# Performance work log

Hardware: AMD Instinct MI355X
Metric: run time of the kernel (lower is better)

Reference implementation:

```python
import jax, jax.numpy as jnp
import numpy as np

B, S, D, H, DFF = 2, 2048, 1024, 16, 4096
DK = D // H
EPS = 1e-6


def setup_inputs() -> dict:
    key = jax.random.key(0)
    ks = jax.random.split(key, 12)
    p = lambda k, shp: (jax.random.normal(k, shp, dtype=jnp.float32) * 0.02)
    return {
        "x": jax.random.normal(ks[0], (B, S, D), dtype=jnp.float32),
        "src_mask": jax.random.randint(ks[1], (B, 1, 1, S), 0, 2, dtype=jnp.int32),
        "wq": p(ks[2], (D, D)), "bq": jnp.zeros((D,), jnp.float32),
        "wk": p(ks[3], (D, D)), "bk": jnp.zeros((D,), jnp.float32),
        "wv": p(ks[4], (D, D)), "bv": jnp.zeros((D,), jnp.float32),
        "wo": p(ks[5], (D, D)), "bo": jnp.zeros((D,), jnp.float32),
        "w1": p(ks[6], (D, DFF)), "b1": jnp.zeros((DFF,), jnp.float32),
        "w2": p(ks[7], (DFF, D)), "b2": jnp.zeros((D,), jnp.float32),
        "a1": jnp.ones((1,), jnp.float32), "g1": jnp.zeros((1,), jnp.float32),
        "a2": jnp.ones((1,), jnp.float32), "g2": jnp.zeros((1,), jnp.float32),
    }


def _layernorm(x, alpha, bias):
    # Faithful to source: scalar alpha/bias, std with Bessel correction, eps on std
    mean = jnp.mean(x, axis=-1, keepdims=True)
    std = jnp.std(x, axis=-1, keepdims=True, ddof=1)
    return alpha * (x - mean) / (std + EPS) + bias


def _encoder_block(x, src_mask, wq, bq, wk, bk, wv, bv, wo, bo,
                   w1, b1, w2, b2, a1, g1, a2, g2):
    # --- self-attention sublayer (pre-norm residual) ---
    n = _layernorm(x, a1, g1)
    q = (n @ wq + bq).reshape(B, S, H, DK)
    k = (n @ wk + bk).reshape(B, S, H, DK)
    v = (n @ wv + bv).reshape(B, S, H, DK)
    scores = jnp.einsum("bqhd,bkhd->bhqk", q, k) / jnp.sqrt(jnp.float32(DK))
    scores = jnp.where(src_mask == 0, jnp.float32(-1e9), scores)
    attn = jax.nn.softmax(scores, axis=-1)
    ctx = jnp.einsum("bhqk,bkhd->bqhd", attn, v).reshape(B, S, D)
    x = x + (ctx @ wo + bo)
    # --- feed-forward sublayer (pre-norm residual) ---
    n2 = _layernorm(x, a2, g2)
    ff = jax.nn.relu(n2 @ w1 + b1) @ w2 + b2
    return x + ff


def reference(x, src_mask, wq, bq, wk, bk, wv, bv, wo, bo,
              w1, b1, w2, b2, a1, g1, a2, g2):
    return _encoder_block(x, src_mask, wq, bq, wk, bk, wv, bv, wo, bo,
                          w1, b1, w2, b2, a1, g1, a2, g2)
```

## Files before the change

### kernel.cpp

```cpp
#include <hip/hip_runtime.h>
#include <hip/hip_bf16.h>
#include <cstdint>

constexpr int Bc  = 2;
constexpr int Sc  = 2048;
constexpr int Dc  = 1024;
constexpr int Hc  = 16;
constexpr int DKc = 64;
constexpr int DFFc= 4096;
constexpr int BSc = Bc * Sc;

typedef __attribute__((ext_vector_type(8))) short bf16x8;
typedef __attribute__((ext_vector_type(4))) float f32x4;

__device__ __forceinline__ unsigned short f2bf(float x){
  union { float f; uint32_t u; } v; v.f = x;
  uint32_t r = v.u + 0x7fffu + ((v.u >> 16) & 1u);
  return (unsigned short)(r >> 16);
}

__device__ __forceinline__ void gload16(const void* g, void* l){
  __builtin_amdgcn_global_load_lds((const __attribute__((address_space(1))) void*)g,
                                   (__attribute__((address_space(3))) void*)l, 16, 0, 0);
}

__device__ __forceinline__ f32x4 mfma16(bf16x8 a, bf16x8 b, f32x4 c){
  return __builtin_amdgcn_mfma_f32_16x16x32_bf16(a, b, c, 0, 0, 0);
}

__device__ __forceinline__ uint32_t pk2bf(float lo, float hi){
  __hip_bfloat162 h = __float22bfloat162_rn(make_float2(lo, hi));
  return *reinterpret_cast<uint32_t*>(&h);
}

__device__ __forceinline__ float fexp2(float x){
  float r; asm("v_exp_f32 %0, %1" : "=v"(r) : "v"(x)); return r;
}

__device__ __forceinline__ int xcd_swz(int bid, int nwg){
  const int q = nwg >> 3, r = nwg & 7;
  const int xcd = bid & 7, idx = bid >> 3;
  return ((xcd < r) ? (xcd * (q + 1)) : (r * (q + 1) + (xcd - r) * q)) + idx;
}

__global__ __launch_bounds__(256)
void prep_all(const float* __restrict__ wq, const float* __restrict__ wk,
              const float* __restrict__ wv, const float* __restrict__ wo,
              const float* __restrict__ w1, const float* __restrict__ w2,
              const float* __restrict__ bq, const float* __restrict__ bk,
              const float* __restrict__ bv,
              unsigned short* __restrict__ wqkv_t, unsigned short* __restrict__ wo_t,
              unsigned short* __restrict__ w1_t, unsigned short* __restrict__ w2_t,
              float* __restrict__ bqkv,
              const float* __restrict__ x, const float* __restrict__ al,
              const float* __restrict__ be, unsigned short* __restrict__ nbuf){
  const int id = blockIdx.x, tid = threadIdx.x;
  if (id >= 12300){
    const int row = id - 12300;
    const float4 v = ((const float4*)(x + (long)row * Dc))[tid];
    float s  = v.x + v.y + v.z + v.w;
    float ss = v.x*v.x + v.y*v.y + v.z*v.z + v.w*v.w;
#pragma unroll
    for (int d = 1; d < 64; d <<= 1){ s += __shfl_xor(s, d, 64); ss += __shfl_xor(ss, d, 64); }
    __shared__ float red[8];
    const int wid = tid >> 6, lane = tid & 63;
    if (lane == 0){ red[wid*2] = s; red[wid*2+1] = ss; }
    __syncthreads();
    s  = red[0] + red[2] + red[4] + red[6];
    ss = red[1] + red[3] + red[5] + red[7];
    const float mean = s * (1.f / 1024.f);
    float var = (ss - s * mean) * (1.f / 1023.f);
    var = fmaxf(var, 0.f);
    const float k = al[0] / (sqrtf(var) + 1e-6f);
    const float g = be[0];
    ushort4 o;
    o.x = f2bf((v.x - mean) * k + g);
    o.y = f2bf((v.y - mean) * k + g);
    o.z = f2bf((v.z - mean) * k + g);
    o.w = f2bf((v.w - mean) * k + g);
    ((ushort4*)(nbuf + (long)row * Dc))[tid] = o;
    return;
  }
  if (id >= 12288){
    const int i = (id - 12288) * 256 + tid;
    bqkv[i] = (i < 1024) ? bq[i] : (i < 2048 ? bk[i - 1024] : bv[i - 2048]);
    return;
  }
  const float* in; unsigned short* out; int K, N, bx, by;
  if (id < 4096){
    const int w = id >> 10, local = id & 1023;
    in  = (w == 0) ? wq : (w == 1) ? wk : (w == 2) ? wv : wo;
    out = (w == 0) ? wqkv_t : (w == 1) ? (wqkv_t + 1048576) : (w == 2) ? (wqkv_t + 2097152) : wo_t;
    K = 1024; N = 1024; bx = local & 31; by = local >> 5;
  } else if (id < 8192){
    const int local = id - 4096;
    in = w1; out = w1_t; K = 1024; N = 4096; bx = local & 127; by = local >> 7;
  } else {
    const int local = id - 8192;
    in = w2; out = w2_t; K = 4096; N = 1024; bx = local & 31; by = local >> 5;
  }
  __shared__ float t[32][33];
  const int tx = tid & 31, ty = tid >> 5;
  const int x0 = bx * 32, y0 = by * 32;
#pragma unroll
  for (int j = ty; j < 32; j += 8) t[j][tx] = in[(long)(y0 + j) * N + x0 + tx];
  __syncthreads();
#pragma unroll
  for (int j = ty; j < 32; j += 8)
    out[(long)(x0 + j) * K + y0 + tx] = f2bf(t[tx][j]);
}

__global__ __launch_bounds__(256)
void layernorm_k(const float* __restrict__ x, const float* __restrict__ al,
                 const float* __restrict__ be, unsigned short* __restrict__ out){
  const int row = blockIdx.x, tid = threadIdx.x;
  const float4 v = ((const float4*)(x + (long)row * Dc))[tid];
  float s  = v.x + v.y + v.z + v.w;
  float ss = v.x*v.x + v.y*v.y + v.z*v.z + v.w*v.w;
#pragma unroll
  for (int d = 1; d < 64; d <<= 1){ s += __shfl_xor(s, d, 64); ss += __shfl_xor(ss, d, 64); }
  __shared__ float red[8];
  const int wid = tid >> 6, lane = tid & 63;
  if (lane == 0){ red[wid*2] = s; red[wid*2+1] = ss; }
  __syncthreads();
  s  = red[0] + red[2] + red[4] + red[6];
  ss = red[1] + red[3] + red[5] + red[7];
  const float mean = s * (1.f / 1024.f);
  float var = (ss - s * mean) * (1.f / 1023.f);
  var = fmaxf(var, 0.f);
  const float k = al[0] / (sqrtf(var) + 1e-6f);
  const float g = be[0];
  ushort4 o;
  o.x = f2bf((v.x - mean) * k + g);
  o.y = f2bf((v.y - mean) * k + g);
  o.z = f2bf((v.z - mean) * k + g);
  o.w = f2bf((v.w - mean) * k + g);
  ((ushort4*)(out + (long)row * Dc))[tid] = o;
}

template<int RELU, int OUTBF16, int RES, int VOUT>
__global__ __launch_bounds__(512, 2)
void gemm256(const unsigned short* __restrict__ A, const unsigned short* __restrict__ BT,
             const float* __restrict__ bias, const float* __restrict__ resid,
             void* __restrict__ Cout, unsigned short* __restrict__ vtw,
             int M, int N, int K){
  __shared__ unsigned short As[2][256 * 64];
  __shared__ unsigned short Bs[2][256 * 64];
  const int tid = threadIdx.x, wid = tid >> 6, lane = tid & 63;
  const int lg = lane >> 4, lr = lane & 15;
  const int wm = wid >> 2, wn = wid & 3;
  const int nwg = gridDim.x * gridDim.y;
  const int wg  = xcd_swz(blockIdx.y * gridDim.x + blockIdx.x, nwg);
  const int bx = wg % gridDim.x, by = wg / gridDim.x;
  const int m0 = by * 256, n0 = bx * 256;
  const long ldA = (long)K * 2;
  const f32x4 zero4 = {0.f, 0.f, 0.f, 0.f};
  f32x4 acc[8][4];
#pragma unroll
  for (int i = 0; i < 8; i++)
#pragma unroll
    for (int j = 0; j < 4; j++) acc[i][j] = zero4;

  auto stage_half = [&](int b, int kt, int h){
    const unsigned short* src = (h < 2) ? A : BT;
    const int rowg = ((h < 2) ? m0 : n0) + (h & 1) * 128;
    char* dst = ((h < 2) ? (char*)As[b] : (char*)Bs[b]) + (h & 1) * 16384;
#pragma unroll
    for (int l = 0; l < 2; ++l){
      const int ob = (wid*2 + l) * 1024;
      const int o  = ob + lane * 16;
      const int rr = o >> 7, c = (o >> 4) & 7;
      const long co = (long)kt * 128 + ((c ^ (rr & 7)) << 4);
      gload16((const char*)src + (long)(rowg + rr) * ldA + co, dst + ob);
    }
  };

  const int nt = K >> 6;
#pragma unroll
  for (int h = 0; h < 4; ++h) stage_half(0, 0, h);
  __syncthreads();

  int cur = 0;
  for (int t = 0; t < nt; ++t){
    const char* as = (const char*)As[cur];
    const char* bs = (const char*)Bs[cur];
    bf16x8 bfr[4][2];
#pragma unroll
    for (int p = 0; p < 4; ++p){
      if (p == 0){
#pragma unroll
        for (int ni = 0; ni < 4; ++ni){
          const int row = wn*64 + ni*16 + lr;
#pragma unroll
          for (int ks = 0; ks < 2; ++ks)
            bfr[ni][ks] = *reinterpret_cast<const bf16x8*>(bs + row*128 + (((ks*4 + lg) ^ (row & 7)) << 4));
        }
      }
      bf16x8 af[2][2];
#pragma unroll
      for (int i = 0; i < 2; ++i){
        const int arow = wm*128 + (2*p + i)*16 + lr;
        af[i][0] = *reinterpret_cast<const bf16x8*>(as + arow*128 + (((0*4 + lg) ^ (arow & 7)) << 4));
        af[i][1] = *reinterpret_cast<const bf16x8*>(as + arow*128 + (((1*4 + lg) ^ (arow & 7)) << 4));
      }
      if (t + 1 < nt) stage_half(cur ^ 1, t + 1, p);
      __builtin_amdgcn_sched_barrier(0);
      __builtin_amdgcn_s_barrier();
      asm volatile("s_waitcnt lgkmcnt(0)" ::: "memory");
      __builtin_amdgcn_sched_barrier(0);
      __builtin_amdgcn_s_setprio(1);
#pragma unroll
      for (int i = 0; i < 2; ++i){
        const int mi = 2*p + i;
#pragma unroll
        for (int ni = 0; ni < 4; ++ni){
          acc[mi][ni] = mfma16(af[i][0], bfr[ni][0], acc[mi][ni]);
          acc[mi][ni] = mfma16(af[i][1], bfr[ni][1], acc[mi][ni]);
        }
      }
      __builtin_amdgcn_s_setprio(0);
      __builtin_amdgcn_sched_barrier(0);
      __builtin_amdgcn_s_barrier();
    }
    if (t + 1 < nt){
      asm volatile("s_waitcnt vmcnt(0)" ::: "memory");
      __builtin_amdgcn_s_barrier();
      __builtin_amdgcn_sched_barrier(0);
    }
    cur ^= 1;
  }

  if (VOUT && n0 >= 2048){
#pragma unroll
    for (int mi = 0; mi < 8; ++mi){
      const int row = m0 + wm*128 + mi*16 + lg*4;
      const int b = row >> 11, s = row & 2047;
#pragma unroll
      for (int ni = 0; ni < 4; ++ni){
        const int col = n0 + wn*64 + ni*16 + lr;
        const float bc = bias[col];
        ushort4 o;
        o.x = f2bf(acc[mi][ni][0] + bc);
        o.y = f2bf(acc[mi][ni][1] + bc);
        o.z = f2bf(acc[mi][ni][2] + bc);
        o.w = f2bf(acc[mi][ni][3] + bc);
        *(ushort4*)(vtw + ((long)(b * 1024 + (col - 2048)) << 11) + s) = o;
      }
    }
    return;
  }

#pragma unroll
  for (int mi = 0; mi < 8; ++mi)
#pragma unroll
    for (int ni = 0; ni < 4; ++ni){
      const int col = n0 + wn*64 + ni*16 + lr;
      const float bc = bias[col];
#pragma unroll
      for (int r = 0; r < 4; ++r){
        const int row = m0 + wm*128 + mi*16 + lg*4 + r;
        float v = acc[mi][ni][r] + bc;
        if (RES)  v += resid[(long)row * N + col];
        if (RELU) v = fmaxf(v, 0.f);
        if (OUTBF16) ((unsigned short*)Cout)[(long)row * N + col] = f2bf(v);
        else         ((float*)Cout)[(long)row * N + col] = v;
      }
    }
}

template<int RELU, int OUTBF16, int RES>
__global__ __launch_bounds__(512, 2)
void gemm12864(const unsigned short* __restrict__ A, const unsigned short* __restrict__ BT,
               const float* __restrict__ bias, const float* __restrict__ resid,
               void* __restrict__ Cout, int M, int N, int K){
  __shared__ unsigned short As[2][128 * 64];
  __shared__ unsigned short Bs[2][64 * 64];
  const int tid = threadIdx.x, wid = tid >> 6, lane = tid & 63;
  const int lg = lane >> 4, lr = lane & 15;
  const int wm = wid >> 1, wn = wid & 1;
  const int nwg = gridDim.x * gridDim.y;
  const int wg  = xcd_swz(blockIdx.y * gridDim.x + blockIdx.x, nwg);
  const int bx = wg % gridDim.x, by = wg / gridDim.x;
  const int m0 = by * 128, n0 = bx * 64;
  const long ldA = (long)K * 2;
  const f32x4 zero4 = {0.f, 0.f, 0.f, 0.f};
  f32x4 acc[2][2];
#pragma unroll
  for (int i = 0; i < 2; i++)
#pragma unroll
    for (int j = 0; j < 2; j++) acc[i][j] = zero4;

  auto stage = [&](int b, int kt){
#pragma unroll
    for (int l = 0; l < 2; ++l){
      const int ob = (wid*2 + l) * 1024;
      const int o  = ob + lane * 16;
      const int rr = o >> 7, c = (o >> 4) & 7;
      const long co = (long)kt * 128 + ((c ^ (rr & 7)) << 4);
      gload16((const char*)A + (long)(m0 + rr) * ldA + co, (char*)As[b] + ob);
    }
    {
      const int ob = wid * 1024;
      const int o  = ob + lane * 16;
      const int rr = o >> 7, c = (o >> 4) & 7;
      const long co = (long)kt * 128 + ((c ^ (rr & 7)) << 4);
      gload16((const char*)BT + (long)(n0 + rr) * ldA + co, (char*)Bs[b] + ob);
    }
  };

  const int nt = K >> 6;
  stage(0, 0);
  stage(1, 1);

  int cur = 0;
  for (int t = 0; t < nt; ++t){
    if (t + 1 < nt) asm volatile("s_waitcnt vmcnt(3)" ::: "memory");
    else            asm volatile("s_waitcnt vmcnt(0)" ::: "memory");
    __builtin_amdgcn_s_barrier();
    __builtin_amdgcn_sched_barrier(0);
    const char* as = (const char*)As[cur];
    const char* bs = (const char*)Bs[cur];
    bf16x8 bfr[2][2];
#pragma unroll
    for (int ni = 0; ni < 2; ++ni){
      const int row = wn*32 + ni*16 + lr;
#pragma unroll
      for (int ks = 0; ks < 2; ++ks)
        bfr[ni][ks] = *reinterpret_cast<const bf16x8*>(bs + row*128 + (((ks*4 + lg) ^ (row & 7)) << 4));
    }
    __builtin_amdgcn_s_setprio(1);
#pragma unroll
    for (int mi = 0; mi < 2; ++mi){
      const int arow = wm*32 + mi*16 + lr;
      bf16x8 a0 = *reinterpret_cast<const bf16x8*>(as + arow*128 + (((0*4 + lg) ^ (arow & 7)) << 4));
      bf16x8 a1 = *reinterpret_cast<const bf16x8*>(as + arow*128 + (((1*4 + lg) ^ (arow & 7)) << 4));
#pragma unroll
      for (int ni = 0; ni < 2; ++ni){
        acc[mi][ni] = mfma16(a0, bfr[ni][0], acc[mi][ni]);
        acc[mi][ni] = mfma16(a1, bfr[ni][1], acc[mi][ni]);
      }
    }
    __builtin_amdgcn_s_setprio(0);
    __builtin_amdgcn_s_barrier();
    __builtin_amdgcn_sched_barrier(0);
    if (t + 2 < nt) stage(cur, t + 2);
    cur ^= 1;
  }

#pragma unroll
  for (int mi = 0; mi < 2; ++mi)
#pragma unroll
    for (int ni = 0; ni < 2; ++ni){
      const int col = n0 + wn*32 + ni*16 + lr;
      const float bc = bias[col];
#pragma unroll
      for (int r = 0; r < 4; ++r){
        const int row = m0 + wm*32 + mi*16 + lg*4 + r;
        float v = acc[mi][ni][r] + bc;
        if (RES)  v += resid[(long)row * N + col];
        if (RELU) v = fmaxf(v, 0.f);
        if (OUTBF16) ((unsigned short*)Cout)[(long)row * N + col] = f2bf(v);
        else         ((float*)Cout)[(long)row * N + col] = v;
      }
    }
}

__global__ __launch_bounds__(512)
void attn_k(const unsigned short* __restrict__ qkv, const unsigned short* __restrict__ vt,
            const int* __restrict__ mask, unsigned short* __restrict__ ctx){
  __shared__ unsigned short QP[128*64], Ks[2][64*64], Vs[2][64*64];
  __shared__ float MAD[2048];
  const int tid = threadIdx.x, wid = tid >> 6, lane = tid & 63;
  const int lg = lane >> 4, lr = lane & 15;
  const int f   = blockIdx.y * gridDim.x + blockIdx.x;
  const int xcd = f & 7, j = f >> 3;
  const int bh  = (xcd << 2) | (j & 3);
  const int qt  = j >> 2;
  const int b = bh >> 4, h = bh & 15;
  const int s0 = qt * 128;
  const f32x4 zero4 = {0.f, 0.f, 0.f, 0.f};
  const short onebf = (short)0x3F80;
  const bf16x8 ones = {onebf, onebf, onebf, onebf, onebf, onebf, onebf, onebf};
  const float c1 = 0.18033688f;

  const char* kbase = (const char*)qkv + (long)(b*Sc) * 6144 + 2048 + h * 128;
  const char* vbase = (const char*)vt + (long)bh * 64 * 4096;
  unsigned short* pb = QP + wid * 1024;

  auto stageKV = [&](int t, int bsel){
    const int o = wid * 1024;
    const int ol = o + lane * 16;
    const int r = ol >> 7, c = (ol >> 4) & 7;
    const int sw = ((c ^ (r & 7)) << 4);
    gload16(kbase + (long)(t*64 + r) * 6144 + sw, (char*)Ks[bsel] + o);
    gload16(vbase + (long)r * 4096 + t*128 + sw, (char*)Vs[bsel] + o);
  };

  const char* qbase = (const char*)qkv + ((long)(b*Sc + s0)) * 6144 + h * 128;
#pragma unroll
  for (int ld = 0; ld < 2; ++ld){
    const int o = (wid*2 + ld) * 1024;
    const int ol = o + lane * 16;
    const int r = ol >> 7, c = (ol >> 4) & 7;
    gload16(qbase + (long)r * 6144 + ((c ^ (r & 7)) << 4), (char*)QP + o);
  }
  stageKV(0, 0);
  {
    const int4 m4 = *(const int4*)(mask + b * Sc + tid * 4);
    float4 fm;
    fm.x = (m4.x != 0) ? 0.f : -1.442695e9f;
    fm.y = (m4.y != 0) ? 0.f : -1.442695e9f;
    fm.z = (m4.z != 0) ? 0.f : -1.442695e9f;
    fm.w = (m4.w != 0) ? 0.f : -1.442695e9f;
    *(float4*)&MAD[tid * 4] = fm;
  }
  __syncthreads();
  bf16x8 qb[2];
#pragma unroll
  for (int ks = 0; ks < 2; ++ks){
    const int row = wid*16 + lr;
    qb[ks] = *reinterpret_cast<const bf16x8*>((const char*)QP + row*128 + (((ks*4 + lg) ^ (row & 7)) << 4));
  }

  f32x4 acc[4] = {zero4, zero4, zero4, zero4};
  f32x4 accS = zero4;
  constexpr int NT = Sc / 64;

  for (int t = 0; t < NT; ++t){
    if (t){
      asm volatile("s_waitcnt vmcnt(0)" ::: "memory");
      __builtin_amdgcn_s_barrier();
      __builtin_amdgcn_sched_barrier(0);
    }
    if (t + 1 < NT) stageKV(t + 1, (t + 1) & 1);

    const int cur = t & 1;
    const int k0 = t * 64;
    const char* ksb = (const char*)Ks[cur];
    const char* vsb = (const char*)Vs[cur];

    f32x4 s4[4];
    __builtin_amdgcn_s_setprio(1);
#pragma unroll
    for (int ni = 0; ni < 4; ++ni){
      s4[ni] = zero4;
      const int row = ni*16 + lr;
#pragma unroll
      for (int ks = 0; ks < 2; ++ks){
        bf16x8 ak = *reinterpret_cast<const bf16x8*>(ksb + row*128 + (((ks*4 + lg) ^ (lr & 7)) << 4));
        s4[ni] = mfma16(ak, qb[ks], s4[ni]);
      }
    }
    __builtin_amdgcn_s_setprio(0);

    float p[4][4];
#pragma unroll
    for (int ni = 0; ni < 4; ++ni){
      const float4 ma = *(const float4*)&MAD[k0 + ni*16 + lg*4];
      p[ni][0] = fexp2(fmaf(s4[ni][0], c1, ma.x));
      p[ni][1] = fexp2(fmaf(s4[ni][1], c1, ma.y));
      p[ni][2] = fexp2(fmaf(s4[ni][2], c1, ma.z));
      p[ni][3] = fexp2(fmaf(s4[ni][3], c1, ma.w));
    }

#pragma unroll
    for (int ni = 0; ni < 4; ++ni){
      uint2 w;
      w.x = pk2bf(p[ni][0], p[ni][1]);
      w.y = pk2bf(p[ni][2], p[ni][3]);
      const int c = ni*2 + (lg >> 1);
      char* dst = (char*)pb + lr*128 + ((c ^ (lr & 7)) << 4) + (lg & 1) * 8;
      *(uint2*)dst = w;
    }
    bf16x8 pa[2];
#pragma unroll
    for (int ks = 0; ks < 2; ++ks){
      pa[ks] = *reinterpret_cast<const bf16x8*>((const char*)pb + lr*128 + (((ks*4 + lg) ^ (lr & 7)) << 4));
    }
    __builtin_amdgcn_s_setprio(1);
#pragma unroll
    for (int ks = 0; ks < 2; ++ks) accS = mfma16(pa[ks], ones, accS);
#pragma unroll
    for (int ni = 0; ni < 4; ++ni){
      const int row = ni*16 + lr;
#pragma unroll
      for (int ks = 0; ks < 2; ++ks){
        bf16x8 bv8 = *reinterpret_cast<const bf16x8*>(vsb + row*128 + (((ks*4 + lg) ^ (lr & 7)) << 4));
        acc[ni] = mfma16(pa[ks], bv8, acc[ni]);
      }
    }
    __builtin_amdgcn_s_setprio(0);
  }
#pragma unroll
  for (int ni = 0; ni < 4; ++ni){
    const int col = h*64 + ni*16 + lr;
#pragma unroll
    for (int r = 0; r < 4; ++r){
      const int row = s0 + wid*16 + lg*4 + r;
      ctx[(long)(b*Sc + row) * Dc + col] = f2bf(acc[ni][r] / accS[r]);
    }
  }
}

extern "C" void kernel_launch(void* const* d_in, const int* in_sizes, int n_in,
                              void* d_out, int out_size, void* d_ws, size_t ws_size,
                              hipStream_t stream){
  const float* x  = (const float*)d_in[0];
  const int* mask = (const int*)d_in[1];
  const float* wq = (const float*)d_in[2];
  const float* bq = (const float*)d_in[3];
  const float* wk = (const float*)d_in[4];
  const float* bk = (const float*)d_in[5];
  const float* wv = (const float*)d_in[6];
  const float* bv = (const float*)d_in[7];
  const float* wo = (const float*)d_in[8];
  const float* bo = (const float*)d_in[9];
  const float* w1 = (const float*)d_in[10];
  const float* b1 = (const float*)d_in[11];
  const float* w2 = (const float*)d_in[12];
  const float* b2 = (const float*)d_in[13];
  const float* a1 = (const float*)d_in[14];
  const float* g1 = (const float*)d_in[15];
  const float* a2 = (const float*)d_in[16];
  const float* g2 = (const float*)d_in[17];

  if (ws_size < 75509760u) return;

  char* ws = (char*)d_ws;
  unsigned short* wqkv_t = (unsigned short*)(ws + 0);
  unsigned short* wo_t   = (unsigned short*)(ws + 6291456);
  unsigned short* w1_t   = (unsigned short*)(ws + 8388608);
  unsigned short* w2_t   = (unsigned short*)(ws + 16777216);
  float*          bqkv   = (float*)(ws + 25165824);
  unsigned short* nbuf   = (unsigned short*)(ws + 25178112);
  unsigned short* qkv    = (unsigned short*)(ws + 33566720);
  unsigned short* ff1    = (unsigned short*)(ws + 33566720);
  unsigned short* vt     = (unsigned short*)(ws + 58732544);
  unsigned short* ctx    = (unsigned short*)(ws + 67121152);
  float* x2 = (float*)d_out;

  prep_all<<<16396, 256, 0, stream>>>(wq, wk, wv, wo, w1, w2, bq, bk, bv,
                                      wqkv_t, wo_t, w1_t, w2_t, bqkv,
                                      x, a1, g1, nbuf);

  gemm256<0,1,0,1><<<dim3(12, 16), 512, 0, stream>>>(nbuf, wqkv_t, bqkv, nullptr, qkv, vt, BSc, 3072, 1024);
  attn_k<<<dim3(16, 32), 512, 0, stream>>>(qkv, vt, mask, ctx);
  gemm12864<0,0,1><<<dim3(16, 32), 512, 0, stream>>>(ctx, wo_t, bo, x, x2, BSc, 1024, 1024);
  layernorm_k<<<BSc, 256, 0, stream>>>(x2, a2, g2, nbuf);
  gemm256<1,1,0,0><<<dim3(16, 16), 512, 0, stream>>>(nbuf, w1_t, b1, nullptr, ff1, nullptr, BSc, 4096, 1024);
  gemm12864<0,0,1><<<dim3(16, 32), 512, 0, stream>>>(ff1, w2_t, b2, x2, d_out, BSc, 1024, 4096);
}
```

Before: 213.7 us.

## Software-pipeline attention: overlap next tile's QK^T with current softmax/PV

Moves the K/V staging to a triple-buffered ring and restructures the attention loop so the QK^T MFMAs for tile t are issued before the exp/pack/PV work of tile t-1. The aim is to let the MFMA pipe overlap the transcendental and LDS round-trip latency within each wave. This costs extra LDS for the third K/V buffer and more live registers for the carried score fragments, which could reduce occupancy or cause register spills.

```diff
diff --git a/kernel.cpp b/kernel.cpp
--- a/kernel.cpp
+++ b/kernel.cpp
@@ -368,7 +368,7 @@
 __global__ __launch_bounds__(512)
 void attn_k(const unsigned short* __restrict__ qkv, const unsigned short* __restrict__ vt,
             const int* __restrict__ mask, unsigned short* __restrict__ ctx){
-  __shared__ unsigned short QP[128*64], Ks[2][64*64], Vs[2][64*64];
+  __shared__ unsigned short QP[128*64], Ks[3][64*64], Vs[3][64*64];
   __shared__ float MAD[2048];
   const int tid = threadIdx.x, wid = tid >> 6, lane = tid & 63;
   const int lg = lane >> 4, lr = lane & 15;
@@ -421,38 +421,31 @@
     const int row = wid*16 + lr;
     qb[ks] = *reinterpret_cast<const bf16x8*>((const char*)QP + row*128 + (((ks*4 + lg) ^ (row & 7)) << 4));
   }
+  stageKV(1, 1);
 
   f32x4 acc[4] = {zero4, zero4, zero4, zero4};
   f32x4 accS = zero4;
   constexpr int NT = Sc / 64;
 
-  for (int t = 0; t < NT; ++t){
-    if (t){
-      asm volatile("s_waitcnt vmcnt(0)" ::: "memory");
-      __builtin_amdgcn_s_barrier();
-      __builtin_amdgcn_sched_barrier(0);
-    }
-    if (t + 1 < NT) stageKV(t + 1, (t + 1) & 1);
-
-    const int cur = t & 1;
-    const int k0 = t * 64;
-    const char* ksb = (const char*)Ks[cur];
-    const char* vsb = (const char*)Vs[cur];
-
-    f32x4 s4[4];
+  f32x4 s4p[4];
+  {
+    const char* ksb = (const char*)Ks[0];
     __builtin_amdgcn_s_setprio(1);
 #pragma unroll
     for (int ni = 0; ni < 4; ++ni){
-      s4[ni] = zero4;
+      s4p[ni] = zero4;
       const int row = ni*16 + lr;
 #pragma unroll
       for (int ks = 0; ks < 2; ++ks){
         bf16x8 ak = *reinterpret_cast<const bf16x8*>(ksb + row*128 + (((ks*4 + lg) ^ (lr & 7)) << 4));
-        s4[ni] = mfma16(ak, qb[ks], s4[ni]);
+        s4p[ni] = mfma16(ak, qb[ks], s4p[ni]);
       }
     }
     __builtin_amdgcn_s_setprio(0);
-
+  }
+
+  auto finish_tile = [&](int tt, const f32x4 (&s4)[4], const char* vsb){
+    const int k0 = tt * 64;
     float p[4][4];
 #pragma unroll
     for (int ni = 0; ni < 4; ++ni){
@@ -462,7 +455,6 @@
       p[ni][2] = fexp2(fmaf(s4[ni][2], c1, ma.z));
       p[ni][3] = fexp2(fmaf(s4[ni][3], c1, ma.w));
     }
-
 #pragma unroll
     for (int ni = 0; ni < 4; ++ni){
       uint2 w;
@@ -490,7 +482,40 @@
       }
     }
     __builtin_amdgcn_s_setprio(0);
-  }
+  };
+
+  int b_prev = 0, b_cur = 1, b_next = 2;
+  for (int t = 1; t < NT; ++t){
+    asm volatile("s_waitcnt vmcnt(0)" ::: "memory");
+    __builtin_amdgcn_s_barrier();
+    __builtin_amdgcn_sched_barrier(0);
+    if (t + 1 < NT) stageKV(t + 1, b_next);
+
+    f32x4 s4n[4];
+    {
+      const char* ksb = (const char*)Ks[b_cur];
+      __builtin_amdgcn_s_setprio(1);
+#pragma unroll
+      for (int ni = 0; ni < 4; ++ni){
+        s4n[ni] = zero4;
+        const int row = ni*16 + lr;
+#pragma unroll
+        for (int ks = 0; ks < 2; ++ks){
+          bf16x8 ak = *reinterpret_cast<const bf16x8*>(ksb + row*128 + (((ks*4 + lg) ^ (lr & 7)) << 4));
+          s4n[ni] = mfma16(ak, qb[ks], s4n[ni]);
+        }
+      }
+      __builtin_amdgcn_s_setprio(0);
+    }
+
+    finish_tile(t - 1, s4p, (const char*)Vs[b_prev]);
+
+#pragma unroll
+    for (int ni = 0; ni < 4; ++ni) s4p[ni] = s4n[ni];
+    const int tmp = b_prev; b_prev = b_cur; b_cur = b_next; b_next = tmp;
+  }
+  finish_tile(NT - 1, s4p, (const char*)Vs[b_prev]);
+
 #pragma unroll
   for (int ni = 0; ni < 4; ++ni){
     const int col = h*64 + ni*16 + lr;
```

After: 216.1 us. About the same (+1.1%).
